# Kernel optimization log

Hardware: AMD Instinct MI355X
Metric: run time of the kernel (lower is better)

## Reference

```python
import jax, jax.numpy as jnp
import numpy as np

DIM = 8       # per-head dim (init arg `dim`)
EPS = 1e-5    # attention normalization eps


def conv2d(x, w, padding, groups=1):
    # x: NCHW, w: OIHW
    return jax.lax.conv_general_dilated(
        x, w, (1, 1), padding, feature_group_count=groups,
        dimension_numbers=('NCHW', 'OIHW', 'NCHW'))


def setup_inputs() -> dict:
    key = jax.random.key(0)
    ks = jax.random.split(key, 12)
    B, Cin, H, W = 16, 256, 64, 64
    hid = 256            # heads(32) * dim(8)
    C3 = hid * 3         # qkv channels = 768
    Ccat = hid * 2       # hidden_dim * (1 + len(scales)) = 512 (post-attn channels)
    Cout = 256
    return {
        'x': jax.random.normal(ks[0], (B, Cin, H, W), jnp.float32),
        'qkv_w': jax.random.normal(ks[1], (C3, Cin, 1, 1), jnp.float32) * 0.05,
        'qkv_bn_scale': jax.random.uniform(ks[2], (C3,), jnp.float32, 0.5, 1.5),
        'qkv_bn_bias': jax.random.normal(ks[3], (C3,), jnp.float32) * 0.1,
        'agg_dw_w': jax.random.normal(ks[4], (C3, 1, 5, 5), jnp.float32) * 0.05,
        'agg_dw_b': jax.random.normal(ks[5], (C3,), jnp.float32) * 0.05,
        'agg_pw_w': jax.random.normal(ks[6], (C3, 1, 1, 1), jnp.float32),
        'agg_pw_b': jax.random.normal(ks[7], (C3,), jnp.float32) * 0.05,
        'proj_w': jax.random.normal(ks[8], (Cout, Ccat, 1, 1), jnp.float32) * 0.05,
        'proj_bn_scale': jax.random.uniform(ks[9], (Cout,), jnp.float32, 0.5, 1.5),
        'proj_bn_bias': jax.random.normal(ks[10], (Cout,), jnp.float32) * 0.1,
    }


def reference(x, qkv_w, qkv_bn_scale, qkv_bn_bias,
              agg_dw_w, agg_dw_b, agg_pw_w, agg_pw_b,
              proj_w, proj_bn_scale, proj_bn_bias):
    B, _, H, W = x.shape
    # qkv = ConvLayer(1x1 conv, eval BN folded to scale/bias, ReLU)
    qkv = conv2d(x, qkv_w, 'SAME')
    qkv = jax.nn.relu(qkv * qkv_bn_scale[:, None, None] + qkv_bn_bias[:, None, None])
    C3 = qkv.shape[1]
    # multi-scale aggregation: depthwise 5x5 (pad 2) + per-channel 1x1, both with bias
    agg = conv2d(qkv, agg_dw_w, [(2, 2), (2, 2)], groups=C3) + agg_dw_b[:, None, None]
    agg = conv2d(agg, agg_pw_w, 'SAME', groups=C3) + agg_pw_b[:, None, None]
    ms = jnp.concatenate([qkv, agg], axis=1)          # (B, 2*C3, H, W)
    # ReLU linear attention (== relu_quadratic_attn math, O(N d^2) form)
    t = ms.reshape(B, -1, 3 * DIM, H * W)             # (B, h, 3d, N), h = 64
    q, k, v = jnp.split(t, 3, axis=2)                 # each (B, h, d, N)
    q = jax.nn.relu(q)
    k = jax.nn.relu(k)
    vk = jnp.einsum('bhdn,bhen->bhde', v, k)          # (B, h, d, d)
    out = jnp.einsum('bhde,bhen->bhdn', vk, q)        # numerator
    denom = jnp.einsum('bhe,bhen->bhn', k.sum(-1), q) # sum_i (k_i . q_j)
    out = out / (denom[:, :, None, :] + EPS)
    out = out.reshape(B, -1, H, W)                    # (B, 512, H, W)
    # proj = ConvLayer(1x1, BN, ReLU)
    out = conv2d(out, proj_w, 'SAME')
    out = jax.nn.relu(out * proj_bn_scale[:, None, None] + proj_bn_bias[:, None, None])
    return out
```

## Files before the change

### kernel.cpp

```cpp
#include <hip/hip_runtime.h>

#define HW    4096
#define WIMG  64
#define CIN   256
#define C3    768
#define COUT  256
#define BATCH 16
#define NHB   32
#define EPS_F 1e-5f
#define QSCALE 1024.0f
#define WSCALE 256.0f

typedef __attribute__((ext_vector_type(8))) short    short8;
typedef __attribute__((ext_vector_type(8))) _Float16 half8;
typedef __attribute__((ext_vector_type(2))) __fp16   fp16x2;
typedef __attribute__((ext_vector_type(4))) float    floatx4;

__device__ inline short f32_to_bf16(float f) {
    unsigned u = __builtin_bit_cast(unsigned, f);
    unsigned r = u + 0x7fffu + ((u >> 16) & 1u);
    return (short)(r >> 16);
}
__device__ inline float bf16_to_f32(short s) {
    return __builtin_bit_cast(float, ((unsigned)(unsigned short)s) << 16);
}

__device__ __forceinline__ void split8_f16(const float* f, half8& hi, half8& lo) {
    #pragma unroll
    for (int p = 0; p < 4; p++) {
        fp16x2 h = __builtin_amdgcn_cvt_pkrtz(f[2 * p], f[2 * p + 1]);
        fp16x2 l = __builtin_amdgcn_cvt_pkrtz(f[2 * p]     - (float)h.x,
                                              f[2 * p + 1] - (float)h.y);
        hi[2 * p] = (_Float16)h.x; hi[2 * p + 1] = (_Float16)h.y;
        lo[2 * p] = (_Float16)l.x; lo[2 * p + 1] = (_Float16)l.y;
    }
}

__device__ __forceinline__ void async_copy_f32(const float* g, float* l) {
    __builtin_amdgcn_global_load_lds(
        (const __attribute__((address_space(1))) void*)g,
        (__attribute__((address_space(3))) void*)l, 4, 0, 0);
}

__global__ __launch_bounds__(256) void conv_q_f32(
    const float* __restrict__ in,
    const float* __restrict__ w,
    const float* __restrict__ scale,
    const float* __restrict__ bias,
    float* __restrict__ Qf)
{
    const int pt  = blockIdx.x * 128;
    const int ct  = blockIdx.y * 64;
    const int b   = blockIdx.z;
    const int tid = threadIdx.x;
    const int lane = tid & 63, wv4 = tid >> 6;
    const int tx  = tid & 15;
    const int ty  = tid >> 4;

    __shared__ float Ws[16][68];
    __shared__ float Xs[16][128];

    float acc[4][8] = {};
    const float* xb = in + (size_t)b * CIN * HW + pt;

    const int c0 = tid >> 2, kq0 = tid & 3;
    const int cp0 = ct + c0;
    const int creal0 = (cp0 >> 3) * 24 + (cp0 & 7);
    const float* wp0 = w + (size_t)creal0 * CIN + kq0 * 4;

    for (int k0 = 0; k0 < CIN; k0 += 16) {
        float4 wa = *reinterpret_cast<const float4*>(wp0 + k0);
        Ws[kq0 * 4 + 0][c0] = wa.x; Ws[kq0 * 4 + 1][c0] = wa.y;
        Ws[kq0 * 4 + 2][c0] = wa.z; Ws[kq0 * 4 + 3][c0] = wa.w;
        #pragma unroll
        for (int r = 0; r < 8; r++) {
            int row  = wv4 * 4 + (r >> 1);
            int half = (r & 1) * 64;
            async_copy_f32(xb + (size_t)(k0 + row) * HW + half + lane,
                           &Xs[row][half]);
        }
        __syncthreads();

        #pragma unroll
        for (int kk = 0; kk < 16; kk++) {
            float4 a0 = *reinterpret_cast<const float4*>(&Ws[kk][ty * 4]);
            float4 b0 = *reinterpret_cast<const float4*>(&Xs[kk][tx * 4]);
            float4 b1 = *reinterpret_cast<const float4*>(&Xs[kk][64 + tx * 4]);
            float a[4] = {a0.x, a0.y, a0.z, a0.w};
            float bb[8] = {b0.x, b0.y, b0.z, b0.w, b1.x, b1.y, b1.z, b1.w};
            #pragma unroll
            for (int i = 0; i < 4; i++)
                #pragma unroll
                for (int j = 0; j < 8; j++)
                    acc[i][j] += a[i] * bb[j];
        }
        __syncthreads();
    }

    #pragma unroll
    for (int i = 0; i < 4; i++) {
        int cp = ct + ty * 4 + i;
        int creal = (cp >> 3) * 24 + (cp & 7);
        float s = scale[creal];
        float bi = bias[creal];
        float4 v0, v1;
        v0.x = fmaxf(acc[i][0] * s + bi, 0.f);
        v0.y = fmaxf(acc[i][1] * s + bi, 0.f);
        v0.z = fmaxf(acc[i][2] * s + bi, 0.f);
        v0.w = fmaxf(acc[i][3] * s + bi, 0.f);
        v1.x = fmaxf(acc[i][4] * s + bi, 0.f);
        v1.y = fmaxf(acc[i][5] * s + bi, 0.f);
        v1.z = fmaxf(acc[i][6] * s + bi, 0.f);
        v1.w = fmaxf(acc[i][7] * s + bi, 0.f);
        float* dst = Qf + ((size_t)b * 256 + cp) * HW + pt;
        *reinterpret_cast<float4*>(dst + tx * 4)      = v0;
        *reinterpret_cast<float4*>(dst + 64 + tx * 4) = v1;
    }
}

__global__ __launch_bounds__(256) void conv_kv_mfma(
    const float* __restrict__ x,
    const float* __restrict__ w,
    const float* __restrict__ scale,
    const float* __restrict__ bias,
    float* __restrict__ KV)
{
    const int ct = blockIdx.x, pt = blockIdx.y, b = blockIdx.z;
    const int tid  = threadIdx.x;
    const int wv   = tid >> 6, lane = tid & 63;
    const int u    = lane & 15, q8 = (lane >> 4) * 8;
    const int chb  = ct * 128 + (wv >> 1) * 64;
    const int pxb  = pt * 128 + (wv & 1) * 64;

    floatx4 acc[4][4];
    #pragma unroll
    for (int i = 0; i < 4; i++)
        #pragma unroll
        for (int j = 0; j < 4; j++) acc[i][j] = (floatx4)0.f;

    for (int kc = 0; kc < 8; kc++) {
        const int k0 = kc * 32 + q8;
        half8 ahi[4], alo[4];
        #pragma unroll
        for (int mt = 0; mt < 4; mt++) {
            int cp = chb + mt * 16 + u;
            int creal = (cp >> 4) * 24 + 8 + (cp & 15);
            const float* wp = w + (size_t)creal * CIN + k0;
            float g[8];
            #pragma unroll
            for (int j = 0; j < 8; j++) g[j] = wp[j] * WSCALE;
            split8_f16(g, ahi[mt], alo[mt]);
        }
        half8 bhi[4], blo[4];
        #pragma unroll
        for (int nt = 0; nt < 4; nt++) {
            const float* xp = x + ((size_t)b * CIN + k0) * HW + pxb + nt * 16 + u;
            float g[8];
            #pragma unroll
            for (int j = 0; j < 8; j++) g[j] = xp[(size_t)j * HW];
            split8_f16(g, bhi[nt], blo[nt]);
        }
        #pragma unroll
        for (int mt = 0; mt < 4; mt++)
            #pragma unroll
            for (int nt = 0; nt < 4; nt++) {
                acc[mt][nt] = __builtin_amdgcn_mfma_f32_16x16x32_f16(ahi[mt], bhi[nt], acc[mt][nt], 0, 0, 0);
                acc[mt][nt] = __builtin_amdgcn_mfma_f32_16x16x32_f16(ahi[mt], blo[nt], acc[mt][nt], 0, 0, 0);
                acc[mt][nt] = __builtin_amdgcn_mfma_f32_16x16x32_f16(alo[mt], bhi[nt], acc[mt][nt], 0, 0, 0);
            }
    }

    const int quad = lane >> 4;
    #pragma unroll
    for (int mt = 0; mt < 4; mt++)
        #pragma unroll
        for (int r = 0; r < 4; r++) {
            int cp = chb + mt * 16 + quad * 4 + r;
            int creal = (cp >> 4) * 24 + 8 + (cp & 15);
            float s = scale[creal] * (1.0f / WSCALE), bi = bias[creal];
            #pragma unroll
            for (int nt = 0; nt < 4; nt++) {
                int px = pxb + nt * 16 + u;
                KV[((size_t)b * 512 + cp) * HW + px] = fmaxf(acc[mt][nt][r] * s + bi, 0.f);
            }
        }
}

__global__ __launch_bounds__(256) void zero_stats(float* __restrict__ stats)
{
    int i = blockIdx.x * 256 + threadIdx.x;
    if (i < BATCH * 64 * 72) stats[i] = 0.f;
}

__global__ __launch_bounds__(256) void attn_stats_direct(
    const float* __restrict__ KV,
    float* __restrict__ stats)
{
    const int h = blockIdx.x, ps = blockIdx.y, b = blockIdx.z;
    const int tid = threadIdx.x;
    const int lane = tid & 63, wv = tid >> 6;
    const int c  = lane & 15;
    const int kg = lane >> 4;

    const float* cb = KV + ((size_t)b * 512 + h * 16 + c) * HW
                    + ps * 1024 + wv * 256 + kg * 8;

    floatx4 accg = (floatx4)0.f;
    floatx4 accs = (floatx4)0.f;
    half8 ones;
    #pragma unroll
    for (int j = 0; j < 8; j++) ones[j] = (_Float16)1.0f;

    for (int st = 0; st < 8; st++) {
        float4 f0 = *reinterpret_cast<const float4*>(cb + st * 32);
        float4 f1 = *reinterpret_cast<const float4*>(cb + st * 32 + 4);
        float v[8] = {f0.x, f0.y, f0.z, f0.w, f1.x, f1.y, f1.z, f1.w};
        half8 hi, lo;
        split8_f16(v, hi, lo);
        accg = __builtin_amdgcn_mfma_f32_16x16x32_f16(hi, hi, accg, 0, 0, 0);
        accg = __builtin_amdgcn_mfma_f32_16x16x32_f16(hi, lo, accg, 0, 0, 0);
        accg = __builtin_amdgcn_mfma_f32_16x16x32_f16(lo, hi, accg, 0, 0, 0);
        accs = __builtin_amdgcn_mfma_f32_16x16x32_f16(hi, ones, accs, 0, 0, 0);
        accs = __builtin_amdgcn_mfma_f32_16x16x32_f16(lo, ones, accs, 0, 0, 0);
    }

    float* sb = stats + ((size_t)b * 64 + h) * 72;
    if (c < 8 && kg >= 2) {
        #pragma unroll
        for (int r = 0; r < 4; r++)
            atomicAdd(sb + ((kg - 2) * 4 + r) * 8 + c, accg[r]);
    }
    if (c == 0 && kg < 2) {
        #pragma unroll
        for (int r = 0; r < 4; r++)
            atomicAdd(sb + 64 + kg * 4 + r, accs[r]);
    }
}

__global__ __launch_bounds__(256) void attn_stats_dw(
    const float* __restrict__ KV,
    const float* __restrict__ dww, const float* __restrict__ dwb,
    const float* __restrict__ pww, const float* __restrict__ pwb,
    float* __restrict__ stats)
{
    const int hp = blockIdx.x, ysb = blockIdx.y, b = blockIdx.z;
    const int tid = threadIdx.x;
    const int lane = tid & 63, wv = tid >> 6;
    const int c  = lane & 15;
    const int kg = lane >> 4;
    const int creal = hp * 24 + 8 + c;

    float wt[25];
    #pragma unroll
    for (int i = 0; i < 25; i++) wt[i] = dww[creal * 25 + i];
    const float pw = pww[creal];
    const float pb = pw * dwb[creal] + pwb[creal];

    const float* cb = KV + ((size_t)b * 512 + hp * 16 + c) * HW;
    const int ybase = ysb * 32 + wv * 8;

    floatx4 accg = (floatx4)0.f;
    floatx4 accs = (floatx4)0.f;
    half8 ones;
    #pragma unroll
    for (int j = 0; j < 8; j++) ones[j] = (_Float16)1.0f;

    #pragma unroll
    for (int xh = 0; xh < 2; xh++) {
        const int x0 = xh * 32 + kg * 8;
        const float mL = (x0 == 0)  ? 0.f : 1.f;
        const float mR = (x0 == 56) ? 0.f : 1.f;
        const int colL = (x0 == 0)  ? 0  : x0 - 4;
        const int colR = (x0 == 56) ? 56 : x0 + 8;

        float out[5][8] = {};
        #pragma unroll
        for (int li = 0; li < 12; li++) {
            const int ry = ybase + li - 2;
            float4 Q0 = {0,0,0,0}, Q1 = {0,0,0,0}, Q2 = {0,0,0,0}, Q3 = {0,0,0,0};
            if (ry >= 0 && ry < WIMG) {
                const float* rp = cb + ry * WIMG;
                Q0 = *reinterpret_cast<const float4*>(rp + colL);
                Q1 = *reinterpret_cast<const float4*>(rp + x0);
                Q2 = *reinterpret_cast<const float4*>(rp + x0 + 4);
                Q3 = *reinterpret_cast<const float4*>(rp + colR);
            }
            float win[12] = {Q0.z * mL, Q0.w * mL,
                             Q1.x, Q1.y, Q1.z, Q1.w,
                             Q2.x, Q2.y, Q2.z, Q2.w,
                             Q3.x * mR, Q3.y * mR};
            #pragma unroll
            for (int rr = 0; rr < 5; rr++) {
                const int lo = li - rr;
                if (lo >= 0 && lo < 8) {
                    #pragma unroll
                    for (int kx = 0; kx < 5; kx++) {
                        float w5 = wt[rr * 5 + kx];
                        #pragma unroll
                        for (int j = 0; j < 8; j++)
                            out[lo % 5][j] += w5 * win[j + kx];
                    }
                }
            }
            const int lod = li - 4;
            if (lod >= 0 && lod < 8) {
                float fv[8];
                #pragma unroll
                for (int j = 0; j < 8; j++) {
                    float v = out[lod % 5][j] * pw + pb;
                    float vr = fmaxf(v, 0.f);
                    fv[j] = (c < 8) ? vr : v;
                }
                half8 hib, lob;
                split8_f16(fv, hib, lob);
                accg = __builtin_amdgcn_mfma_f32_16x16x32_f16(hib, hib, accg, 0, 0, 0);
                accg = __builtin_amdgcn_mfma_f32_16x16x32_f16(hib, lob, accg, 0, 0, 0);
                accg = __builtin_amdgcn_mfma_f32_16x16x32_f16(lob, hib, accg, 0, 0, 0);
                accs = __builtin_amdgcn_mfma_f32_16x16x32_f16(hib, ones, accs, 0, 0, 0);
                accs = __builtin_amdgcn_mfma_f32_16x16x32_f16(lob, ones, accs, 0, 0, 0);
                #pragma unroll
                for (int j = 0; j < 8; j++) out[lod % 5][j] = 0.f;
            }
        }
    }

    float* sb = stats + ((size_t)b * 64 + 32 + hp) * 72;
    if (c < 8 && kg >= 2) {
        #pragma unroll
        for (int r = 0; r < 4; r++)
            atomicAdd(sb + ((kg - 2) * 4 + r) * 8 + c, accg[r]);
    }
    if (c == 0 && kg < 2) {
        #pragma unroll
        for (int r = 0; r < 4; r++)
            atomicAdd(sb + 64 + kg * 4 + r, accs[r]);
    }
}

__global__ __launch_bounds__(256) void q_dwconv(
    const float* __restrict__ Qf,
    const float* __restrict__ dww, const float* __restrict__ dwb,
    const float* __restrict__ pww, const float* __restrict__ pwb,
    float* __restrict__ Qagg)
{
    const int hb = blockIdx.x, ysb = blockIdx.y, b = blockIdx.z;
    const int tid = threadIdx.x;
    const int lane = tid & 63, wv = tid >> 6;
    const int c = lane & 7;
    const int g = lane >> 3;
    const int x0 = g * 8;
    const int creal = hb * 24 + c;

    float wt[25];
    #pragma unroll
    for (int i = 0; i < 25; i++) wt[i] = dww[creal * 25 + i];
    const float pw = pww[creal];
    const float pb = pw * dwb[creal] + pwb[creal];

    const float mL = (x0 == 0)  ? 0.f : 1.f;
    const float mR = (x0 == 56) ? 0.f : 1.f;
    const int colL = (x0 == 0)  ? 0  : x0 - 4;
    const int colR = (x0 == 56) ? 56 : x0 + 8;

    const float* cbase = Qf   + ((size_t)b * 256 + hb * 8 + c) * HW;
    float*       obase = Qagg + ((size_t)b * 256 + hb * 8 + c) * HW;
    const int ybase = ysb * 32 + wv * 8;

    float out[5][8] = {};
    #pragma unroll
    for (int li = 0; li < 12; li++) {
        const int ry = ybase + li - 2;
        float4 Q0 = {0,0,0,0}, Q1 = {0,0,0,0}, Q2 = {0,0,0,0}, Q3 = {0,0,0,0};
        if (ry >= 0 && ry < WIMG) {
            const float* rp = cbase + ry * WIMG;
            Q0 = *reinterpret_cast<const float4*>(rp + colL);
            Q1 = *reinterpret_cast<const float4*>(rp + x0);
            Q2 = *reinterpret_cast<const float4*>(rp + x0 + 4);
            Q3 = *reinterpret_cast<const float4*>(rp + colR);
        }
        float win[12] = {Q0.z * mL, Q0.w * mL,
                         Q1.x, Q1.y, Q1.z, Q1.w,
                         Q2.x, Q2.y, Q2.z, Q2.w,
                         Q3.x * mR, Q3.y * mR};
        #pragma unroll
        for (int rr = 0; rr < 5; rr++) {
            const int lo = li - rr;
            if (lo >= 0 && lo < 8) {
                #pragma unroll
                for (int kx = 0; kx < 5; kx++) {
                    float w5 = wt[rr * 5 + kx];
                    #pragma unroll
                    for (int j = 0; j < 8; j++)
                        out[lo % 5][j] += w5 * win[j + kx];
                }
            }
        }
        const int lod = li - 4;
        if (lod >= 0 && lod < 8) {
            float4 o0 = {out[lod % 5][0] * pw + pb, out[lod % 5][1] * pw + pb,
                         out[lod % 5][2] * pw + pb, out[lod % 5][3] * pw + pb};
            float4 o1 = {out[lod % 5][4] * pw + pb, out[lod % 5][5] * pw + pb,
                         out[lod % 5][6] * pw + pb, out[lod % 5][7] * pw + pb};
            float* dst = obase + (ybase + lod) * WIMG + x0;
            *reinterpret_cast<float4*>(dst)     = o0;
            *reinterpret_cast<float4*>(dst + 4) = o1;
            #pragma unroll
            for (int j = 0; j < 8; j++) out[lod % 5][j] = 0.f;
        }
    }
}

__global__ __launch_bounds__(256) void build_M(
    const float* __restrict__ stats,
    const float* __restrict__ projw,
    _Float16* __restrict__ Mhi,
    _Float16* __restrict__ Mlo)
{
    const int hg = blockIdx.x;
    const int b  = blockIdx.y;
    const int tid = threadIdx.x;

    __shared__ float svk[8][64];
    __shared__ float sginv[8][8];

    for (int i = tid; i < 8 * 64; i += 256) {
        int h = i >> 6;
        svk[h][i & 63] = stats[((size_t)b * 64 + hg * 8 + h) * 72 + (i & 63)];
    }
    if (tid < 64)
        sginv[tid >> 3][tid & 7] =
            1.0f / (stats[((size_t)b * 64 + hg * 8 + (tid >> 3)) * 72 + 64 + (tid & 7)] + EPS_F);
    __syncthreads();

    const float* wr = projw + (size_t)tid * 512 + hg * 64;
    #pragma unroll
    for (int hh = 0; hh < 8; hh++) {
        float wv[8];
        float4 a0 = *reinterpret_cast<const float4*>(wr + hh * 8);
        float4 a1 = *reinterpret_cast<const float4*>(wr + hh * 8 + 4);
        wv[0]=a0.x; wv[1]=a0.y; wv[2]=a0.z; wv[3]=a0.w;
        wv[4]=a1.x; wv[5]=a1.y; wv[6]=a1.z; wv[7]=a1.w;
        union { _Float16 h8[8]; uint4 u; } hi, lo;
        #pragma unroll
        for (int e = 0; e < 8; e++) {
            float s = 0.f;
            #pragma unroll
            for (int d = 0; d < 8; d++) s += wv[d] * svk[hh][d * 8 + e];
            s *= sginv[hh][e];
            _Float16 sh = (_Float16)s;
            hi.h8[e] = sh;
            lo.h8[e] = (_Float16)(s - (float)sh);
        }
        size_t off = ((size_t)b * 256 + tid) * 512 + hg * 64 + hh * 8;
        *reinterpret_cast<uint4*>(Mhi + off) = hi.u;
        *reinterpret_cast<uint4*>(Mlo + off) = lo.u;
    }
}

__global__ __launch_bounds__(256) void attn_proj_mfma(
    const float* __restrict__ Qf,
    const float* __restrict__ Qagg,
    const float* __restrict__ stats,
    const _Float16* __restrict__ Mhi,
    const _Float16* __restrict__ Mlo,
    const float* __restrict__ scale, const float* __restrict__ bias,
    float* __restrict__ out)
{
    const int pt  = blockIdx.x * 128;
    const int b   = blockIdx.y;
    const int tid = threadIdx.x;
    const int wv  = tid >> 6, lane = tid & 63;

    __shared__ _Float16 Qt[128][264];
    __shared__ float    ksums[64][8];

    for (int i = tid; i < 512; i += 256)
        ksums[i >> 3][i & 7] = stats[((size_t)b * 64 + (i >> 3)) * 72 + 64 + (i & 7)];
    __syncthreads();

    const int pxl = tid & 127;
    const int eg  = (tid >> 7) * 4;
    const int u = lane & 15, q8 = (lane >> 4) * 8;
    const int quad = lane >> 4;

    floatx4 acc[4][8];
    #pragma unroll
    for (int i = 0; i < 4; i++)
        #pragma unroll
        for (int j = 0; j < 8; j++) acc[i][j] = (floatx4)0.f;

    for (int h = 0; h < 32; h++) {
        const float* qp = Qf + ((size_t)b * 256 + h * 8) * HW + pt + pxl;
        float qv[8];
        #pragma unroll
        for (int e = 0; e < 8; e++) qv[e] = qp[(size_t)e * HW];
        float den = EPS_F;
        #pragma unroll
        for (int e = 0; e < 8; e++) den += ksums[h][e] * qv[e];
        float rd = QSCALE / den;
        union { _Float16 h4[4]; uint2 u2; } pk;
        #pragma unroll
        for (int j = 0; j < 4; j++) {
            float g = ksums[h][eg + j] + EPS_F;
            pk.h4[j] = (_Float16)fminf(qv[eg + j] * g * rd, 60000.f);
        }
        *reinterpret_cast<uint2*>(&Qt[pxl][h * 8 + eg]) = pk.u2;
    }
    __syncthreads();

    for (int ks = 0; ks < 8; ks++) {
        half8 ah[4], al[4], bf[8];
        #pragma unroll
        for (int mt = 0; mt < 4; mt++) {
            size_t moff = ((size_t)b * 256 + wv * 64 + mt * 16 + u) * 512 + ks * 32 + q8;
            ah[mt] = *reinterpret_cast<const half8*>(Mhi + moff);
            al[mt] = *reinterpret_cast<const half8*>(Mlo + moff);
        }
        #pragma unroll
        for (int nt = 0; nt < 8; nt++)
            bf[nt] = *reinterpret_cast<const half8*>(&Qt[nt * 16 + u][ks * 32 + q8]);
        #pragma unroll
        for (int mt = 0; mt < 4; mt++)
            #pragma unroll
            for (int nt = 0; nt < 8; nt++) {
                acc[mt][nt] = __builtin_amdgcn_mfma_f32_16x16x32_f16(ah[mt], bf[nt], acc[mt][nt], 0, 0, 0);
                acc[mt][nt] = __builtin_amdgcn_mfma_f32_16x16x32_f16(al[mt], bf[nt], acc[mt][nt], 0, 0, 0);
            }
    }
    __syncthreads();

    for (int h = 32; h < 64; h++) {
        const int hb = h - 32;
        const float* qp = Qagg + ((size_t)b * 256 + hb * 8) * HW + pt + pxl;
        float qv[8];
        #pragma unroll
        for (int e = 0; e < 8; e++) qv[e] = fmaxf(qp[(size_t)e * HW], 0.f);
        float den = EPS_F;
        #pragma unroll
        for (int e = 0; e < 8; e++) den += ksums[h][e] * qv[e];
        float rd = QSCALE / den;
        union { _Float16 h4[4]; uint2 u2; } pk;
        #pragma unroll
        for (int j = 0; j < 4; j++) {
            float g = ksums[h][eg + j] + EPS_F;
            pk.h4[j] = (_Float16)fminf(qv[eg + j] * g * rd, 60000.f);
        }
        *reinterpret_cast<uint2*>(&Qt[pxl][hb * 8 + eg]) = pk.u2;
    }
    __syncthreads();

    for (int ks = 0; ks < 8; ks++) {
        half8 ah[4], al[4], bf[8];
        #pragma unroll
        for (int mt = 0; mt < 4; mt++) {
            size_t moff = ((size_t)b * 256 + wv * 64 + mt * 16 + u) * 512 + 256 + ks * 32 + q8;
            ah[mt] = *reinterpret_cast<const half8*>(Mhi + moff);
            al[mt] = *reinterpret_cast<const half8*>(Mlo + moff);
        }
        #pragma unroll
        for (int nt = 0; nt < 8; nt++)
            bf[nt] = *reinterpret_cast<const half8*>(&Qt[nt * 16 + u][ks * 32 + q8]);
        #pragma unroll
        for (int mt = 0; mt < 4; mt++)
            #pragma unroll
            for (int nt = 0; nt < 8; nt++) {
                acc[mt][nt] = __builtin_amdgcn_mfma_f32_16x16x32_f16(ah[mt], bf[nt], acc[mt][nt], 0, 0, 0);
                acc[mt][nt] = __builtin_amdgcn_mfma_f32_16x16x32_f16(al[mt], bf[nt], acc[mt][nt], 0, 0, 0);
            }
    }

    #pragma unroll
    for (int mt = 0; mt < 4; mt++)
        #pragma unroll
        for (int r = 0; r < 4; r++) {
            int c = wv * 64 + mt * 16 + quad * 4 + r;
            float s = scale[c] * (1.0f / QSCALE);
            float bi = bias[c];
            #pragma unroll
            for (int nt = 0; nt < 8; nt++) {
                int px = pt + nt * 16 + u;
                out[((size_t)b * COUT + c) * HW + px] = fmaxf(acc[mt][nt][r] * s + bi, 0.f);
            }
        }
}

extern "C" void kernel_launch(void* const* d_in, const int* in_sizes, int n_in,
                              void* d_out, int out_size, void* d_ws, size_t ws_size,
                              hipStream_t stream)
{
    const float* x      = (const float*)d_in[0];
    const float* qkv_w  = (const float*)d_in[1];
    const float* qkv_s  = (const float*)d_in[2];
    const float* qkv_b  = (const float*)d_in[3];
    const float* dw_w   = (const float*)d_in[4];
    const float* dw_b   = (const float*)d_in[5];
    const float* pw_w   = (const float*)d_in[6];
    const float* pw_b   = (const float*)d_in[7];
    const float* proj_w = (const float*)d_in[8];
    const float* proj_s = (const float*)d_in[9];
    const float* proj_b = (const float*)d_in[10];
    float* out = (float*)d_out;

    float*    KV    = (float*)d_ws;
    _Float16* Mhi   = (_Float16*)d_ws;
    _Float16* Mlo   = Mhi + (size_t)BATCH * 256 * 512;
    float*    Qagg  = (float*)(Mlo + (size_t)BATCH * 256 * 512);
    float*    Qf    = KV + (size_t)BATCH * 512 * HW;
    float*    stats = Qf + (size_t)BATCH * 256 * HW;

    conv_q_f32<<<dim3(HW / 128, 4, BATCH), 256, 0, stream>>>(
        x, qkv_w, qkv_s, qkv_b, Qf);

    conv_kv_mfma<<<dim3(4, 32, BATCH), 256, 0, stream>>>(
        x, qkv_w, qkv_s, qkv_b, KV);

    zero_stats<<<dim3((BATCH * 64 * 72 + 255) / 256), 256, 0, stream>>>(stats);

    attn_stats_direct<<<dim3(32, 4, BATCH), 256, 0, stream>>>(KV, stats);

    attn_stats_dw<<<dim3(32, 2, BATCH), 256, 0, stream>>>(
        KV, dw_w, dw_b, pw_w, pw_b, stats);

    q_dwconv<<<dim3(32, 2, BATCH), 256, 0, stream>>>(
        Qf, dw_w, dw_b, pw_w, pw_b, Qagg);

    build_M<<<dim3(8, BATCH), 256, 0, stream>>>(stats, proj_w, Mhi, Mlo);

    attn_proj_mfma<<<dim3(HW / 128, BATCH), 256, 0, stream>>>(
        Qf, Qagg, stats, Mhi, Mlo, proj_s, proj_b, out);
}
```

Baseline: 570.6 us.

## Chunk attention-proj K loop into 8-head phases with smaller LDS tile

Restructures the attention+projection kernel to build and consume Q in eight phases of 8 heads (64 K columns) instead of two phases of 32 heads, shrinking the shared Qt tile from 128x264 to 128x72 halves. The smaller LDS footprint is meant to let more blocks reside per CU, raising occupancy so global loads overlap with MFMA work. In exchange it adds more __syncthreads barriers per block and a per-head branch between Qf and Qagg sources.

```diff
diff --git a/kernel.cpp b/kernel.cpp
--- a/kernel.cpp
+++ b/kernel.cpp
@@ -471,7 +471,7 @@
     const int tid = threadIdx.x;
     const int wv  = tid >> 6, lane = tid & 63;
 
-    __shared__ _Float16 Qt[128][264];
+    __shared__ _Float16 Qt[128][72];
     __shared__ float    ksums[64][8];
 
     for (int i = tid; i < 512; i += 256)
@@ -489,84 +489,58 @@
         #pragma unroll
         for (int j = 0; j < 8; j++) acc[i][j] = (floatx4)0.f;
 
-    for (int h = 0; h < 32; h++) {
-        const float* qp = Qf + ((size_t)b * 256 + h * 8) * HW + pt + pxl;
-        float qv[8];
-        #pragma unroll
-        for (int e = 0; e < 8; e++) qv[e] = qp[(size_t)e * HW];
-        float den = EPS_F;
-        #pragma unroll
-        for (int e = 0; e < 8; e++) den += ksums[h][e] * qv[e];
-        float rd = QSCALE / den;
-        union { _Float16 h4[4]; uint2 u2; } pk;
-        #pragma unroll
-        for (int j = 0; j < 4; j++) {
-            float g = ksums[h][eg + j] + EPS_F;
-            pk.h4[j] = (_Float16)fminf(qv[eg + j] * g * rd, 60000.f);
-        }
-        *reinterpret_cast<uint2*>(&Qt[pxl][h * 8 + eg]) = pk.u2;
-    }
-    __syncthreads();
-
-    for (int ks = 0; ks < 8; ks++) {
-        half8 ah[4], al[4], bf[8];
-        #pragma unroll
-        for (int mt = 0; mt < 4; mt++) {
-            size_t moff = ((size_t)b * 256 + wv * 64 + mt * 16 + u) * 512 + ks * 32 + q8;
-            ah[mt] = *reinterpret_cast<const half8*>(Mhi + moff);
-            al[mt] = *reinterpret_cast<const half8*>(Mlo + moff);
-        }
-        #pragma unroll
-        for (int nt = 0; nt < 8; nt++)
-            bf[nt] = *reinterpret_cast<const half8*>(&Qt[nt * 16 + u][ks * 32 + q8]);
-        #pragma unroll
-        for (int mt = 0; mt < 4; mt++)
-            #pragma unroll
-            for (int nt = 0; nt < 8; nt++) {
-                acc[mt][nt] = __builtin_amdgcn_mfma_f32_16x16x32_f16(ah[mt], bf[nt], acc[mt][nt], 0, 0, 0);
-                acc[mt][nt] = __builtin_amdgcn_mfma_f32_16x16x32_f16(al[mt], bf[nt], acc[mt][nt], 0, 0, 0);
-            }
-    }
-    __syncthreads();
-
-    for (int h = 32; h < 64; h++) {
-        const int hb = h - 32;
-        const float* qp = Qagg + ((size_t)b * 256 + hb * 8) * HW + pt + pxl;
-        float qv[8];
-        #pragma unroll
-        for (int e = 0; e < 8; e++) qv[e] = fmaxf(qp[(size_t)e * HW], 0.f);
-        float den = EPS_F;
-        #pragma unroll
-        for (int e = 0; e < 8; e++) den += ksums[h][e] * qv[e];
-        float rd = QSCALE / den;
-        union { _Float16 h4[4]; uint2 u2; } pk;
-        #pragma unroll
-        for (int j = 0; j < 4; j++) {
-            float g = ksums[h][eg + j] + EPS_F;
-            pk.h4[j] = (_Float16)fminf(qv[eg + j] * g * rd, 60000.f);
-        }
-        *reinterpret_cast<uint2*>(&Qt[pxl][hb * 8 + eg]) = pk.u2;
-    }
-    __syncthreads();
-
-    for (int ks = 0; ks < 8; ks++) {
-        half8 ah[4], al[4], bf[8];
-        #pragma unroll
-        for (int mt = 0; mt < 4; mt++) {
-            size_t moff = ((size_t)b * 256 + wv * 64 + mt * 16 + u) * 512 + 256 + ks * 32 + q8;
-            ah[mt] = *reinterpret_cast<const half8*>(Mhi + moff);
-            al[mt] = *reinterpret_cast<const half8*>(Mlo + moff);
-        }
-        #pragma unroll
-        for (int nt = 0; nt < 8; nt++)
-            bf[nt] = *reinterpret_cast<const half8*>(&Qt[nt * 16 + u][ks * 32 + q8]);
-        #pragma unroll
-        for (int mt = 0; mt < 4; mt++)
-            #pragma unroll
-            for (int nt = 0; nt < 8; nt++) {
-                acc[mt][nt] = __builtin_amdgcn_mfma_f32_16x16x32_f16(ah[mt], bf[nt], acc[mt][nt], 0, 0, 0);
-                acc[mt][nt] = __builtin_amdgcn_mfma_f32_16x16x32_f16(al[mt], bf[nt], acc[mt][nt], 0, 0, 0);
-            }
+    #pragma unroll 1
+    for (int ph = 0; ph < 8; ph++) {
+        const int h0 = ph * 8;
+        #pragma unroll
+        for (int hh = 0; hh < 8; hh++) {
+            const int h = h0 + hh;
+            float qv[8];
+            if (h < 32) {
+                const float* qp = Qf + ((size_t)b * 256 + h * 8) * HW + pt + pxl;
+                #pragma unroll
+                for (int e = 0; e < 8; e++) qv[e] = qp[(size_t)e * HW];
+            } else {
+                const float* qp = Qagg + ((size_t)b * 256 + (h - 32) * 8) * HW + pt + pxl;
+                #pragma unroll
+                for (int e = 0; e < 8; e++) qv[e] = fmaxf(qp[(size_t)e * HW], 0.f);
+            }
+            float den = EPS_F;
+            #pragma unroll
+            for (int e = 0; e < 8; e++) den += ksums[h][e] * qv[e];
+            float rd = QSCALE / den;
+            union { _Float16 h4[4]; uint2 u2; } pk;
+            #pragma unroll
+            for (int j = 0; j < 4; j++) {
+                float g = ksums[h][eg + j] + EPS_F;
+                pk.h4[j] = (_Float16)fminf(qv[eg + j] * g * rd, 60000.f);
+            }
+            *reinterpret_cast<uint2*>(&Qt[pxl][hh * 8 + eg]) = pk.u2;
+        }
+        __syncthreads();
+
+        #pragma unroll
+        for (int ks = 0; ks < 2; ks++) {
+            half8 ah[4], al[4], bf[8];
+            #pragma unroll
+            for (int mt = 0; mt < 4; mt++) {
+                size_t moff = ((size_t)b * 256 + wv * 64 + mt * 16 + u) * 512
+                            + ph * 64 + ks * 32 + q8;
+                ah[mt] = *reinterpret_cast<const half8*>(Mhi + moff);
+                al[mt] = *reinterpret_cast<const half8*>(Mlo + moff);
+            }
+            #pragma unroll
+            for (int nt = 0; nt < 8; nt++)
+                bf[nt] = *reinterpret_cast<const half8*>(&Qt[nt * 16 + u][ks * 32 + q8]);
+            #pragma unroll
+            for (int mt = 0; mt < 4; mt++)
+                #pragma unroll
+                for (int nt = 0; nt < 8; nt++) {
+                    acc[mt][nt] = __builtin_amdgcn_mfma_f32_16x16x32_f16(ah[mt], bf[nt], acc[mt][nt], 0, 0, 0);
+                    acc[mt][nt] = __builtin_amdgcn_mfma_f32_16x16x32_f16(al[mt], bf[nt], acc[mt][nt], 0, 0, 0);
+                }
+        }
+        __syncthreads();
     }
 
     #pragma unroll
```

After: 569.8 us. Within noise of the previous version (-0.1%).
